# Kernel optimization log

Hardware: AMD Instinct MI355X
Metric: run time of the kernel (lower is better)

## Reference

```python
import jax, jax.numpy as jnp
import numpy as np
from jax import lax

DIM = 128
HEADS = 8
GROUPS = 8
DIM_HEAD = 64
DOWN = 4
OFF_SCALE = 4.0
KSIZE = 6
B, N, M = 2, 1024, 1024


def ln(x, g, b, eps=1e-5):
    m = x.mean(-1, keepdims=True)
    v = ((x - m) ** 2).mean(-1, keepdims=True)
    return (x - m) / jnp.sqrt(v + eps) * g + b


def grid_sample_1d(feats, grid):
    # feats: (Bg, C, Mk), grid: (Bg, Nd) normalized coords in [-1, 1]
    # bilinear, padding_mode='zeros', align_corners=False (torch semantics)
    Bg, C, Mk = feats.shape
    x = ((grid + 1.0) * Mk - 1.0) / 2.0
    x0 = jnp.floor(x)
    w1 = x - x0

    def gather(xi):
        valid = ((xi >= 0) & (xi <= Mk - 1)).astype(feats.dtype)
        idx = jnp.clip(xi, 0, Mk - 1).astype(jnp.int32)
        vals = jnp.take_along_axis(
            feats, jnp.broadcast_to(idx[:, None, :], (Bg, C, idx.shape[-1])), axis=2)
        return vals * valid[:, None, :]

    return gather(x0) * (1.0 - w1)[:, None, :] + gather(x0 + 1.0) * w1[:, None, :]


def deform_cross_attn(xq, xkv, qw, kw, vw, ow, ob, o1w, o1b, o2w,
                      c1w, c1b, c2w, c2b, c3w, c3b):
    # xq, xkv: (B, C, N) channel-first token streams
    Bb, C, Nq = xq.shape
    cg = C // GROUPS  # 16 channels per offset group
    q = jnp.einsum('bgcn,goc->bgon', xq.reshape(Bb, GROUPS, cg, Nq), qw)  # (B,g,64,N)
    gq = q.reshape(Bb * GROUPS, DIM_HEAD, Nq)
    pad = (KSIZE - DOWN) // 2
    off = lax.conv_general_dilated(gq, o1w[:, None, :], (DOWN,), [(pad, pad)],
                                   feature_group_count=DIM_HEAD,
                                   dimension_numbers=('NCH', 'OIH', 'NCH')) + o1b[None, :, None]
    off = jax.nn.gelu(off, approximate=False)
    off = jnp.tanh(jnp.einsum('bcn,c->bn', off, o2w)) * OFF_SCALE  # (B*g, Nd)
    Nd = off.shape[-1]
    vgrid = jnp.arange(Nd, dtype=off.dtype)[None] + off
    vgs = 2.0 * vgrid / max(Nd - 1, 1) - 1.0  # normalized sample positions
    xkv_g = xkv.reshape(Bb, GROUPS, cg, xkv.shape[-1]).reshape(Bb * GROUPS, cg, xkv.shape[-1])
    kv = grid_sample_1d(xkv_g, vgs).reshape(Bb, GROUPS, cg, Nd)
    k = jnp.einsum('bgcn,goc->bgon', kv, kw)
    v = jnp.einsum('bgcn,goc->bgon', kv, vw)
    sim = jnp.einsum('bhdi,bhdj->bhij', q * (DIM_HEAD ** -0.5), k)  # heads == groups
    seq = 2.0 * jnp.arange(Nq, dtype=vgs.dtype) / max(Nq - 1, 1) - 1.0
    rel = seq[None, :, None] - vgs[:, None, :]  # (B*g, N, Nd)
    bias = jnp.sign(rel) * jnp.log1p(jnp.abs(rel))
    h = jax.nn.relu(bias[..., None] * c1w[0] + c1b)  # CPB MLP, hidden=dim//4=32
    h = jax.nn.relu(h @ c2w + c2b)
    h = (h @ c3w + c3b)[..., 0]
    sim = sim + h.reshape(Bb, GROUPS, Nq, Nd)  # heads // offset_groups == 1
    attn = jax.nn.softmax(sim, axis=-1)
    out = jnp.einsum('bhij,bhdj->bhdi', attn, v).reshape(Bb, GROUPS * DIM_HEAD, Nq)
    out = jnp.einsum('bcn,oc->bon', out, ow) + ob[:, None]
    return out, attn


def mha(q_in, kv_in, w_in, b_in, w_out, b_out):
    # seq-first torch nn.MultiheadAttention, eval mode (no dropout)
    E = DIM; h = HEADS; dh = E // h
    q = q_in @ w_in[:E].T + b_in[:E]
    k = kv_in @ w_in[E:2 * E].T + b_in[E:2 * E]
    v = kv_in @ w_in[2 * E:].T + b_in[2 * E:]
    Lq, Bb, _ = q.shape
    Lk = k.shape[0]
    qh = q.reshape(Lq, Bb, h, dh).transpose(1, 2, 0, 3)
    kh = k.reshape(Lk, Bb, h, dh).transpose(1, 2, 0, 3)
    vh = v.reshape(Lk, Bb, h, dh).transpose(1, 2, 0, 3)
    attn = jax.nn.softmax(jnp.einsum('bhid,bhjd->bhij', qh, kh) * (dh ** -0.5), axis=-1)
    out = jnp.einsum('bhij,bhjd->bhid', attn, vh).transpose(2, 0, 1, 3).reshape(Lq, Bb, E)
    return out @ w_out.T + b_out


def transfusion(x1, x2, ng, nb, inw, inb, ow, ob, pw, pb):
    x = x1 + mha(ln(x1, ng, nb), ln(x2, ng, nb), inw, inb, ow, ob)
    x = ln(x.transpose(1, 0, 2), ng, nb)  # (B, N, E)
    return jnp.tanh(x.mean(1) @ pw.T + pb)[:, None, :]  # (B, 1, E)


def setup_inputs():
    key = jax.random.key(0)
    ks = iter(jax.random.split(key, 40))
    rn = lambda shape, s=0.05: jax.random.normal(next(ks), shape, dtype=jnp.float32) * s
    return {
        'x1_0': rn((B, N, DIM), 1.0),
        'x1_1': rn((B, N, DIM), 1.0),
        'x2': rn((B, M, DIM), 1.0),
        'norm_g': jnp.ones((DIM,), jnp.float32),
        'norm_b': jnp.zeros((DIM,), jnp.float32),
        'd_qw': rn((2, GROUPS, DIM_HEAD, DIM // GROUPS)),
        'd_kw': rn((2, GROUPS, DIM_HEAD, DIM // GROUPS)),
        'd_vw': rn((2, GROUPS, DIM_HEAD, DIM // GROUPS)),
        'd_ow': rn((2, DIM, GROUPS * DIM_HEAD)),
        'd_ob': jnp.zeros((2, DIM), jnp.float32),
        'd_off1w': rn((2, DIM_HEAD, KSIZE)),
        'd_off1b': jnp.zeros((2, DIM_HEAD), jnp.float32),
        'd_off2w': rn((2, DIM_HEAD)),
        'd_cpb_w1': rn((2, 1, 32)),
        'd_cpb_b1': jnp.zeros((2, 32), jnp.float32),
        'd_cpb_w2': rn((2, 32, 32)),
        'd_cpb_b2': jnp.zeros((2, 32), jnp.float32),
        'd_cpb_w3': rn((2, 32, 1)),
        'd_cpb_b3': jnp.zeros((2, 1), jnp.float32),
        'fus_w': rn((DIM, 2 * DIM)),
        'fus_b': jnp.zeros((DIM,), jnp.float32),
        'tf_ng': jnp.ones((2, DIM), jnp.float32),
        'tf_nb': jnp.zeros((2, DIM), jnp.float32),
        'tf_inw': rn((2, 3 * DIM, DIM)),
        'tf_inb': jnp.zeros((2, 3 * DIM), jnp.float32),
        'tf_ow': rn((2, DIM, DIM)),
        'tf_ob': jnp.zeros((2, DIM), jnp.float32),
        'tf_pw': rn((2, DIM, DIM)),
        'tf_pb': jnp.zeros((2, DIM), jnp.float32),
        'attn_dim': 128,
    }


def reference(x1_0, x1_1, x2, norm_g, norm_b, d_qw, d_kw, d_vw, d_ow, d_ob,
              d_off1w, d_off1b, d_off2w, d_cpb_w1, d_cpb_b1, d_cpb_w2, d_cpb_b2,
              d_cpb_w3, d_cpb_b3, fus_w, fus_b, tf_ng, tf_nb, tf_inw, tf_inb,
              tf_ow, tf_ob, tf_pw, tf_pb, attn_dim):
    nkv = ln(x2, norm_g, norm_b).transpose(0, 2, 1)
    xo1, a1 = deform_cross_attn(ln(x1_0, norm_g, norm_b).transpose(0, 2, 1), nkv,
                                d_qw[0], d_kw[0], d_vw[0], d_ow[0], d_ob[0],
                                d_off1w[0], d_off1b[0], d_off2w[0],
                                d_cpb_w1[0], d_cpb_b1[0], d_cpb_w2[0], d_cpb_b2[0],
                                d_cpb_w3[0], d_cpb_b3[0])
    xo2, a2 = deform_cross_attn(ln(x1_1, norm_g, norm_b).transpose(0, 2, 1), nkv,
                                d_qw[1], d_kw[1], d_vw[1], d_ow[1], d_ob[1],
                                d_off1w[1], d_off1b[1], d_off2w[1],
                                d_cpb_w1[1], d_cpb_b1[1], d_cpb_w2[1], d_cpb_b2[1],
                                d_cpb_w3[1], d_cpb_b3[1])
    xout1 = x1_0 + xo1.transpose(0, 2, 1)
    xout2 = x1_1 + xo2.transpose(0, 2, 1)
    x = jnp.concatenate([xout1, xout2], axis=-1) @ fus_w.T + fus_b
    query = ln(x, norm_g, norm_b).transpose(1, 0, 2)
    kv1 = ln(x1_0[:, :1, :], norm_g, norm_b).transpose(1, 0, 2)
    kv2 = ln(x1_1[:, :1, :], norm_g, norm_b).transpose(1, 0, 2)
    f1 = transfusion(query, kv1, tf_ng[0], tf_nb[0], tf_inw[0], tf_inb[0],
                     tf_ow[0], tf_ob[0], tf_pw[0], tf_pb[0])
    f2 = transfusion(query, kv2, tf_ng[1], tf_nb[1], tf_inw[1], tf_inb[1],
                     tf_ow[1], tf_ob[1], tf_pw[1], tf_pb[1])
    return (f1, f2, a1, a2)
```

## Files before the change

kernel.cpp:

```cpp
#include <hip/hip_runtime.h>
#include <hip/hip_bf16.h>


namespace {

constexpr int kN  = 1024;
constexpr int kC  = 128;
constexpr int kG  = 8;
constexpr int kDH = 64;
constexpr int kND = 256;

constexpr int   kNT    = 2048;
constexpr float kRLO   = -2.0625f;
constexpr float kRSPAN = 4.125f;

constexpr size_t W_LNKV = 0;
constexpr size_t W_LNQ1 = 262144;
constexpr size_t W_LNQ2 = 524288;
constexpr size_t W_Q    = 786432;
constexpr size_t W_K    = 1835008;
constexpr size_t W_VT   = 2097152;
constexpr size_t W_VGS  = 2359296;
constexpr size_t W_AO   = 2367488;
constexpr size_t W_TAB  = 5251072;
constexpr size_t W_MOUT = 5283844;
constexpr size_t W_PART = 5284356;
constexpr size_t W_OWB  = 5317124;
constexpr size_t W_FWB  = 5382660;

}

typedef __attribute__((ext_vector_type(8))) short short8;
typedef __attribute__((ext_vector_type(4))) float floatx4;

__device__ __forceinline__ float wave_sum(float v) {
#pragma unroll
  for (int o = 32; o > 0; o >>= 1) v += __shfl_xor(v, o, 64);
  return v;
}
__device__ __forceinline__ float cpb_lds(const float* __restrict__ tabL,
                                         float seq, float vg) {
  float rel = seq - vg;
  float ft = (rel - kRLO) * ((float)kNT / kRSPAN);
  ft = fminf(fmaxf(ft, 0.f), (float)kNT - 0.001f);
  int ix = (int)ft;
  float fw = ft - (float)ix;
  return tabL[ix] * (1.f - fw) + tabL[ix + 1] * fw;
}

__global__ void k_prep(const float* __restrict__ ow, const float* __restrict__ fw,
                       __hip_bfloat16* __restrict__ owb, __hip_bfloat16* __restrict__ fwb,
                       const float* __restrict__ x1_0, const float* __restrict__ x1_1,
                       const float* __restrict__ x2, float* __restrict__ lnq1,
                       float* __restrict__ lnq2, float* __restrict__ lnkv,
                       const float* __restrict__ ng, const float* __restrict__ nb,
                       const float* __restrict__ cw1, const float* __restrict__ cb1,
                       const float* __restrict__ cw2, const float* __restrict__ cb2,
                       const float* __restrict__ cw3, const float* __restrict__ cb3,
                       float* __restrict__ tab,
                       const float* __restrict__ tfng, const float* __restrict__ tfnb,
                       const float* __restrict__ inw, const float* __restrict__ inb,
                       const float* __restrict__ tow, const float* __restrict__ tob,
                       float* __restrict__ mout) {
  int bx = blockIdx.x;
  int t = threadIdx.x;
  if (bx < 640) {
    int id = bx * 256 + t;
    if (id < 131072) owb[id] = __float2bfloat16(ow[id]);
    else fwb[id - 131072] = __float2bfloat16(fw[id - 131072]);
  } else if (bx < 2176) {
    int w = t >> 6, lane = t & 63;
    int gr = (bx - 640) * 4 + w;
    int sel = gr >> 11, row = gr & 2047;
    const float* in = (sel == 0) ? x1_0 : (sel == 1) ? x1_1 : x2;
    float* out = (sel == 0) ? lnq1 : (sel == 1) ? lnq2 : lnkv;
    const float* xr = in + (size_t)row * kC;
    float xa = xr[lane], xb = xr[lane + 64];
    float m = wave_sum(xa + xb) * (1.f / kC);
    float da = xa - m, db = xb - m;
    float v = wave_sum(da * da + db * db) * (1.f / kC);
    float r = rsqrtf(v + 1e-5f);
    float* orow = out + (size_t)row * kC;
    orow[lane]      = da * r * ng[lane] + nb[lane];
    orow[lane + 64] = db * r * ng[lane + 64] + nb[lane + 64];
  } else if (bx < 2194) {
    int rel = bx - 2176;
    int idx = rel / 9, bb = rel - idx * 9;
    int tt = bb * 256 + t;
    if (tt <= kNT) {
      float rel_ = kRLO + (kRSPAN / (float)kNT) * (float)tt;
      float u = (rel_ >= 0.f ? 1.f : -1.f) * log1pf(fabsf(rel_));
      const float* W1 = cw1 + idx * 32; const float* B1 = cb1 + idx * 32;
      const float* W2 = cw2 + idx * 1024; const float* B2 = cb2 + idx * 32;
      const float* W3 = cw3 + idx * 32; const float* B3 = cb3 + idx;
      float h1[32];
#pragma unroll
      for (int m = 0; m < 32; ++m) h1[m] = fmaxf(0.f, u * W1[m] + B1[m]);
      float o = B3[0];
      for (int m = 0; m < 32; ++m) {
        float a = B2[m];
#pragma unroll
        for (int k = 0; k < 32; ++k) a += h1[k] * W2[k * 32 + m];
        o += fmaxf(a, 0.f) * W3[m];
      }
      tab[(size_t)idx * (kNT + 1) + tt] = o;
    }
  } else {
    int rel = bx - 2194;
    int i = rel >> 1, b = rel & 1;
    bool act = t < 128;
    __shared__ float red[2];
    __shared__ float s1[128];
    __shared__ float s2[128];
    const float* xs = (i ? x1_1 : x1_0) + (size_t)b * kN * kC;
    float x = act ? xs[t] : 0.f;
    float s = wave_sum(x);
    if (act && (t & 63) == 0) red[t >> 6] = s;
    __syncthreads();
    float m1 = (red[0] + red[1]) * (1.f / kC);
    __syncthreads();
    float d1 = x - m1;
    float ss = wave_sum(act ? d1 * d1 : 0.f);
    if (act && (t & 63) == 0) red[t >> 6] = ss;
    __syncthreads();
    float v1 = (red[0] + red[1]) * (1.f / kC);
    __syncthreads();
    float t0 = act ? d1 * rsqrtf(v1 + 1e-5f) * ng[t] + nb[t] : 0.f;
    s = wave_sum(t0);
    if (act && (t & 63) == 0) red[t >> 6] = s;
    __syncthreads();
    float m2 = (red[0] + red[1]) * (1.f / kC);
    __syncthreads();
    float d2 = t0 - m2;
    ss = wave_sum(act ? d2 * d2 : 0.f);
    if (act && (t & 63) == 0) red[t >> 6] = ss;
    __syncthreads();
    float v2 = (red[0] + red[1]) * (1.f / kC);
    if (act) s1[t] = d2 * rsqrtf(v2 + 1e-5f) * tfng[i * kC + t] + tfnb[i * kC + t];
    __syncthreads();
    if (act) {
      float a0 = 0.f;
      const float* wr = inw + (size_t)i * 384 * kC + (size_t)(256 + t) * kC;
      for (int c = 0; c < 128; ++c) a0 += s1[c] * wr[c];
      s2[t] = inb[i * 384 + 256 + t] + a0;
    }
    __syncthreads();
    if (act) {
      float a0 = 0.f;
      const float* wr2 = tow + (size_t)i * kC * kC + (size_t)t * kC;
      for (int c = 0; c < 128; ++c) a0 += s2[c] * wr2[c];
      mout[rel * kC + t] = tob[i * kC + t] + a0;
    }
  }
}

__global__ void k_qoff(const float* __restrict__ lnq1, const float* __restrict__ lnq2,
                       const float* __restrict__ qw, const float* __restrict__ o1w,
                       const float* __restrict__ o1b, const float* __restrict__ o2w,
                       __hip_bfloat16* __restrict__ qout, float* __restrict__ vgs) {
  int bx = blockIdx.x;
  if (bx < 512) {
    int bg = bx >> 4, r0 = (bx & 15) * 64;
    int str = bg >> 4, b = (bg >> 3) & 1, g = bg & 7;
    int rl = threadIdx.x & 63, dq = threadIdx.x >> 6;
    const float* lnq = str ? lnq2 : lnq1;
    const float* xr = lnq + ((size_t)(b * kN + r0 + rl)) * kC + g * 16;
    float4 x0 = *(const float4*)(xr + 0);
    float4 x1 = *(const float4*)(xr + 4);
    float4 x2 = *(const float4*)(xr + 8);
    float4 x3 = *(const float4*)(xr + 12);
    const float* wqb = qw + (size_t)str * 8192 + (size_t)g * 1024;
    __hip_bfloat16* qrow = qout + ((size_t)bg * 1024 + r0 + rl) * 64 + dq * 16;
#pragma unroll 4
    for (int dd = 0; dd < 16; ++dd) {
      int d = dq * 16 + dd;
      const float* wq = wqb + d * 16;
      float4 w0 = *(const float4*)(wq + 0);
      float4 w1 = *(const float4*)(wq + 4);
      float4 w2 = *(const float4*)(wq + 8);
      float4 w3 = *(const float4*)(wq + 12);
      float q = x0.x * w0.x + x0.y * w0.y + x0.z * w0.z + x0.w * w0.w
              + x1.x * w1.x + x1.y * w1.y + x1.z * w1.z + x1.w * w1.w
              + x2.x * w2.x + x2.y * w2.y + x2.z * w2.z + x2.w * w2.w
              + x3.x * w3.x + x3.y * w3.y + x3.z * w3.z + x3.w * w3.w;
      qrow[dd] = __float2bfloat16(q);
    }
  } else {
    int bxo = bx - 512;
    int w = threadIdx.x >> 6, lane = threadIdx.x & 63;
    int bg = bxo >> 6, j = ((bxo & 63) << 2) + w;
    int str = bg >> 4, b = (bg >> 3) & 1, g = bg & 7;
    const float* lnq = str ? lnq2 : lnq1;
    __shared__ float xr[4][96];
    int base = j * 4 - 1;
#pragma unroll
    for (int rep = 0; rep < 2; ++rep) {
      int idx = lane + rep * 64;
      if (idx < 96) {
        int r = idx >> 4, c = idx & 15, n = base + r;
        xr[w][idx] = (n >= 0 && n < kN)
                         ? lnq[((size_t)(b * kN + n)) * kC + g * 16 + c] : 0.f;
      }
    }
    const float* wq = qw + (size_t)str * 8192 + (size_t)(g * kDH + lane) * 16;
    float acc = o1b[str * 64 + lane];
#pragma unroll
    for (int k2 = 0; k2 < 6; ++k2) {
      float qv = 0.f;
#pragma unroll
      for (int c = 0; c < 16; ++c) qv += xr[w][k2 * 16 + c] * wq[c];
      acc += qv * o1w[str * 384 + lane * 6 + k2];
    }
    float ge = 0.5f * acc * (1.f + erff(acc * 0.70710678118654752440f));
    float s = wave_sum(ge * o2w[str * 64 + lane]);
    if (lane == 0)
      vgs[bg * kND + j] = 2.f * ((float)j + tanhf(s) * 4.0f) / 255.f - 1.f;
  }
}

__global__ void k_sample_kv(const float* __restrict__ lnkv, const float* __restrict__ vgs,
                            const float* __restrict__ kw, const float* __restrict__ vw,
                            __hip_bfloat16* __restrict__ kout,
                            __hip_bfloat16* __restrict__ vtout) {
  int w = threadIdx.x >> 6, lane = threadIdx.x & 63;
  int bg = blockIdx.x >> 6, j = ((blockIdx.x & 63) << 2) + w;
  int str = bg >> 4, b = (bg >> 3) & 1, g = bg & 7;
  __shared__ float sc[4][16];
  if (lane < 16) {
    float gr = vgs[bg * kND + j];
    float x = ((gr + 1.f) * 1024.f - 1.f) * 0.5f;
    float x0f = floorf(x);
    float w1 = x - x0f;
    int x0 = (int)x0f, x1 = x0 + 1;
    const float* src = lnkv + (size_t)b * kN * kC + g * 16 + lane;
    float v0 = (x0 >= 0 && x0 < 1024) ? src[(size_t)x0 * kC] : 0.f;
    float v1 = (x1 >= 0 && x1 < 1024) ? src[(size_t)x1 * kC] : 0.f;
    sc[w][lane] = v0 * (1.f - w1) + v1 * w1;
  }
  const float* kwr = kw + (size_t)str * 8192 + (size_t)(g * kDH + lane) * 16;
  const float* vwr = vw + (size_t)str * 8192 + (size_t)(g * kDH + lane) * 16;
  float ka = 0.f, va = 0.f;
#pragma unroll
  for (int c = 0; c < 16; ++c) { ka += sc[w][c] * kwr[c]; va += sc[w][c] * vwr[c]; }
  kout[((size_t)bg * 256 + j) * 64 + lane] = __float2bfloat16(ka);
  vtout[((size_t)bg * 64 + lane) * 256 + j] = __float2bfloat16(va);
}

__global__ void __launch_bounds__(256, 2)
k_attn(const __hip_bfloat16* __restrict__ q_g, const __hip_bfloat16* __restrict__ k_g,
       const __hip_bfloat16* __restrict__ vt_g, const float* __restrict__ vgs,
       const float* __restrict__ tab, float* __restrict__ aout,
       __hip_bfloat16* __restrict__ attout) {
  int bg = blockIdx.x >> 4, tile = blockIdx.x & 15;
  int str = bg >> 4;
  int i0 = tile * 64;
  int t = threadIdx.x;
  int w = t >> 6, l = t & 63;
  int lr = l & 15, lg = l >> 4;

  __shared__ __align__(16) __hip_bfloat16 Qs[64 * 72];
  __shared__ __align__(16) __hip_bfloat16 Ss[64 * 72];
  __shared__ __align__(16) __hip_bfloat16 Ps[64 * 264];

  const float* tabs = tab + str * (kNT + 1);

  {
    int r = t >> 2, c0 = (t & 3) * 16;
    const __hip_bfloat16* src = q_g + ((size_t)bg * 1024 + i0 + r) * 64 + c0;
    *(float4*)&Qs[r * 72 + c0]     = *(const float4*)src;
    *(float4*)&Qs[r * 72 + c0 + 8] = *(const float4*)(src + 8);
  }
  short8 a0 = *(const short8*)&Qs[(w * 16 + lr) * 72 + lg * 8];
  short8 a1 = *(const short8*)&Qs[(w * 16 + lr) * 72 + 32 + lg * 8];
  __syncthreads();
  float* tabL = (float*)Qs;
  for (int e = t; e <= kNT; e += 256) tabL[e] = tabs[e];

  floatx4 acc[16];
#pragma unroll
  for (int f = 0; f < 16; ++f) acc[f] = {0.f, 0.f, 0.f, 0.f};

#pragma unroll
  for (int jc = 0; jc < 4; ++jc) {
    __syncthreads();
    {
      int r = t >> 2, c0 = (t & 3) * 16;
      const __hip_bfloat16* src = k_g + ((size_t)bg * 256 + jc * 64 + r) * 64 + c0;
      *(float4*)&Ss[r * 72 + c0]     = *(const float4*)src;
      *(float4*)&Ss[r * 72 + c0 + 8] = *(const float4*)(src + 8);
    }
    __syncthreads();
#pragma unroll
    for (int ct = 0; ct < 4; ++ct) {
      short8 b0 = *(const short8*)&Ss[(ct * 16 + lr) * 72 + lg * 8];
      short8 b1 = *(const short8*)&Ss[(ct * 16 + lr) * 72 + 32 + lg * 8];
      acc[jc * 4 + ct] =
          __builtin_amdgcn_mfma_f32_16x16x32_bf16(a0, b0, acc[jc * 4 + ct], 0, 0, 0);
      acc[jc * 4 + ct] =
          __builtin_amdgcn_mfma_f32_16x16x32_bf16(a1, b1, acc[jc * 4 + ct], 0, 0, 0);
    }
  }

  float vgl[16];
#pragma unroll
  for (int f = 0; f < 16; ++f) vgl[f] = vgs[bg * 256 + f * 16 + lr];
  float* aoutb = aout + (size_t)str * 4194304 + (size_t)(bg & 15) * 262144;
#pragma unroll
  for (int reg = 0; reg < 4; ++reg) {
    int row = w * 16 + lg * 4 + reg;
    int i = i0 + row;
    float seq = 2.f * (float)i / 1023.f - 1.f;
    float sv[16];
#pragma unroll
    for (int f = 0; f < 16; ++f)
      sv[f] = acc[f][reg] * 0.125f + cpb_lds(tabL, seq, vgl[f]);
    float m = sv[0];
#pragma unroll
    for (int f = 1; f < 16; ++f) m = fmaxf(m, sv[f]);
    m = fmaxf(m, __shfl_xor(m, 1, 64));
    m = fmaxf(m, __shfl_xor(m, 2, 64));
    m = fmaxf(m, __shfl_xor(m, 4, 64));
    m = fmaxf(m, __shfl_xor(m, 8, 64));
    float ev[16], sum = 0.f;
#pragma unroll
    for (int f = 0; f < 16; ++f) { ev[f] = expf(sv[f] - m); sum += ev[f]; }
    sum += __shfl_xor(sum, 1, 64);
    sum += __shfl_xor(sum, 2, 64);
    sum += __shfl_xor(sum, 4, 64);
    sum += __shfl_xor(sum, 8, 64);
    float inv = 1.f / sum;
    float* arow = aoutb + (size_t)i * 256;
#pragma unroll
    for (int f = 0; f < 16; ++f) {
      float p = ev[f] * inv;
      arow[f * 16 + lr] = p;
      Ps[row * 264 + f * 16 + lr] = __float2bfloat16(p);
    }
  }

  floatx4 oacc[4];
#pragma unroll
  for (int dt = 0; dt < 4; ++dt) oacc[dt] = {0.f, 0.f, 0.f, 0.f};
#pragma unroll
  for (int jc = 0; jc < 4; ++jc) {
    __syncthreads();
    {
      int r = t >> 2, c0 = (t & 3) * 16;
      const __hip_bfloat16* src = vt_g + ((size_t)bg * 64 + r) * 256 + jc * 64 + c0;
      *(float4*)&Ss[r * 72 + c0]     = *(const float4*)src;
      *(float4*)&Ss[r * 72 + c0 + 8] = *(const float4*)(src + 8);
    }
    __syncthreads();
    short8 pa0 = *(const short8*)&Ps[(w * 16 + lr) * 264 + jc * 64 + lg * 8];
    short8 pa1 = *(const short8*)&Ps[(w * 16 + lr) * 264 + jc * 64 + 32 + lg * 8];
#pragma unroll
    for (int dt = 0; dt < 4; ++dt) {
      short8 b0 = *(const short8*)&Ss[(dt * 16 + lr) * 72 + lg * 8];
      short8 b1 = *(const short8*)&Ss[(dt * 16 + lr) * 72 + 32 + lg * 8];
      oacc[dt] = __builtin_amdgcn_mfma_f32_16x16x32_bf16(pa0, b0, oacc[dt], 0, 0, 0);
      oacc[dt] = __builtin_amdgcn_mfma_f32_16x16x32_bf16(pa1, b1, oacc[dt], 0, 0, 0);
    }
  }
  {
    int b = (bg >> 3) & 1, g = bg & 7;
    __hip_bfloat16* ab = attout + ((size_t)(str * 2 + b) * 1024) * 512 + (size_t)g * 64;
#pragma unroll
    for (int dt = 0; dt < 4; ++dt)
#pragma unroll
      for (int reg = 0; reg < 4; ++reg) {
        int row = w * 16 + lg * 4 + reg;
        ab[(size_t)(i0 + row) * 512 + dt * 16 + lr] = __float2bfloat16(oacc[dt][reg]);
      }
  }
}

__global__ void __launch_bounds__(256, 2)
k_oproj_fuse(const __hip_bfloat16* __restrict__ aog, const __hip_bfloat16* __restrict__ owb,
             const float* __restrict__ ob,
             const float* __restrict__ x1_0, const float* __restrict__ x1_1,
             const __hip_bfloat16* __restrict__ fwb, const float* __restrict__ fb,
             const float* __restrict__ ng, const float* __restrict__ nb,
             const float* __restrict__ tfng, const float* __restrict__ tfnb,
             const float* __restrict__ mout, float* __restrict__ partial) {
  int tok0 = blockIdx.x * 16;
  int t = threadIdx.x;
  int w = t >> 6, l = t & 63;
  int lr = l & 15, lg = l >> 4;
  int nt0 = w * 2;

  __shared__ __align__(16) unsigned char smem[16 * 280 * 2];
  __shared__ float red[4][128];
  __hip_bfloat16* xos = (__hip_bfloat16*)smem;
  float* fs = (float*)smem;

  for (int s = 0; s < 2; ++s) {
    const __hip_bfloat16* arow = aog + ((size_t)(s * 2048 + tok0 + lr)) * 512 + lg * 8;
    const __hip_bfloat16* wb0 = owb + (size_t)s * 65536 + (size_t)((nt0 + 0) * 16 + lr) * 512 + lg * 8;
    const __hip_bfloat16* wb1 = owb + (size_t)s * 65536 + (size_t)((nt0 + 1) * 16 + lr) * 512 + lg * 8;
    floatx4 acc0 = {0.f, 0.f, 0.f, 0.f}, acc1 = {0.f, 0.f, 0.f, 0.f};
#pragma unroll
    for (int ks = 0; ks < 16; ++ks) {
      short8 a  = *(const short8*)(arow + ks * 32);
      short8 b0 = *(const short8*)(wb0 + ks * 32);
      short8 b1 = *(const short8*)(wb1 + ks * 32);
      acc0 = __builtin_amdgcn_mfma_f32_16x16x32_bf16(a, b0, acc0, 0, 0, 0);
      acc1 = __builtin_amdgcn_mfma_f32_16x16x32_bf16(a, b1, acc1, 0, 0, 0);
    }
    const float* x1 = s ? x1_1 : x1_0;
    float bias0 = ob[s * 128 + nt0 * 16 + lr];
    float bias1 = ob[s * 128 + (nt0 + 1) * 16 + lr];
#pragma unroll
    for (int reg = 0; reg < 4; ++reg) {
      int row = lg * 4 + reg;
      size_t xi = (size_t)(tok0 + row) * 128;
      xos[row * 280 + s * 128 + nt0 * 16 + lr] =
          __float2bfloat16(acc0[reg] + x1[xi + nt0 * 16 + lr] + bias0);
      xos[row * 280 + s * 128 + (nt0 + 1) * 16 + lr] =
          __float2bfloat16(acc1[reg] + x1[xi + (nt0 + 1) * 16 + lr] + bias1);
    }
  }
  __syncthreads();

  floatx4 f0 = {0.f, 0.f, 0.f, 0.f}, f1 = {0.f, 0.f, 0.f, 0.f};
  const __hip_bfloat16* fb0 = fwb + (size_t)((nt0 + 0) * 16 + lr) * 256 + lg * 8;
  const __hip_bfloat16* fb1 = fwb + (size_t)((nt0 + 1) * 16 + lr) * 256 + lg * 8;
#pragma unroll
  for (int ks = 0; ks < 8; ++ks) {
    short8 a  = *(const short8*)&xos[lr * 280 + ks * 32 + lg * 8];
    short8 b0 = *(const short8*)(fb0 + ks * 32);
    short8 b1 = *(const short8*)(fb1 + ks * 32);
    f0 = __builtin_amdgcn_mfma_f32_16x16x32_bf16(a, b0, f0, 0, 0, 0);
    f1 = __builtin_amdgcn_mfma_f32_16x16x32_bf16(a, b1, f1, 0, 0, 0);
  }
  __syncthreads();

  {
    float fbias0 = fb[nt0 * 16 + lr], fbias1 = fb[(nt0 + 1) * 16 + lr];
#pragma unroll
    for (int reg = 0; reg < 4; ++reg) {
      int row = lg * 4 + reg;
      fs[row * 132 + w * 32 + lr]      = f0[reg] + fbias0;
      fs[row * 132 + w * 32 + 16 + lr] = f1[reg] + fbias1;
    }
  }
  __syncthreads();

  int b = tok0 >> 10, chunk = (tok0 & 1023) >> 4;
  float g1a = ng[l], b1a = nb[l], g1b = ng[l + 64], b1b = nb[l + 64];
  float mo0a = mout[b * 128 + l], mo0b = mout[b * 128 + l + 64];
  float mo1a = mout[(2 + b) * 128 + l], mo1b = mout[(2 + b) * 128 + l + 64];
  float g20a = tfng[l], b20a = tfnb[l], g20b = tfng[l + 64], b20b = tfnb[l + 64];
  float g21a = tfng[128 + l], b21a = tfnb[128 + l];
  float g21b = tfng[192 + l], b21b = tfnb[192 + l];
  float acc0a = 0.f, acc0b = 0.f, acc1a = 0.f, acc1b = 0.f;
#pragma unroll
  for (int it = 0; it < 4; ++it) {
    int tok = it * 4 + w;
    float xa = fs[tok * 132 + l], xb = fs[tok * 132 + l + 64];
    float m1 = wave_sum(xa + xb) * (1.f / kC);
    float da = xa - m1, db = xb - m1;
    float v1 = wave_sum(da * da + db * db) * (1.f / kC);
    float r1 = rsqrtf(v1 + 1e-5f);
    float ba = da * r1 * g1a + b1a, bb = db * r1 * g1b + b1b;
    {
      float za = ba + mo0a, zb = bb + mo0b;
      float m2 = wave_sum(za + zb) * (1.f / kC);
      float ea = za - m2, eb = zb - m2;
      float v2 = wave_sum(ea * ea + eb * eb) * (1.f / kC);
      float r2 = rsqrtf(v2 + 1e-5f);
      acc0a += ea * r2 * g20a + b20a;
      acc0b += eb * r2 * g20b + b20b;
    }
    {
      float za = ba + mo1a, zb = bb + mo1b;
      float m2 = wave_sum(za + zb) * (1.f / kC);
      float ea = za - m2, eb = zb - m2;
      float v2 = wave_sum(ea * ea + eb * eb) * (1.f / kC);
      float r2 = rsqrtf(v2 + 1e-5f);
      acc1a += ea * r2 * g21a + b21a;
      acc1b += eb * r2 * g21b + b21b;
    }
  }
  red[w][l] = acc0a; red[w][l + 64] = acc0b;
  __syncthreads();
  if (w == 0) {
    float* pr = partial + ((size_t)(b)*64 + chunk) * kC;
    pr[l]      = red[0][l] + red[1][l] + red[2][l] + red[3][l];
    pr[l + 64] = red[0][l + 64] + red[1][l + 64] + red[2][l + 64] + red[3][l + 64];
  }
  __syncthreads();
  red[w][l] = acc1a; red[w][l + 64] = acc1b;
  __syncthreads();
  if (w == 0) {
    float* pr = partial + ((size_t)(2 + b) * 64 + chunk) * kC;
    pr[l]      = red[0][l] + red[1][l] + red[2][l] + red[3][l];
    pr[l + 64] = red[0][l + 64] + red[1][l + 64] + red[2][l + 64] + red[3][l + 64];
  }
}

__global__ void k_final(const float* __restrict__ partial, const float* __restrict__ pw,
                        const float* __restrict__ pb, float* __restrict__ out) {
  int ib = blockIdx.x;
  int i = ib >> 1, t = threadIdx.x;
  int c = t & 127, half = t >> 7;
  float a = 0.f;
  for (int ch = half * 32; ch < half * 32 + 32; ++ch)
    a += partial[((size_t)ib * 64 + ch) * kC + c];
  __shared__ float s[256];
  s[half * 128 + c] = a;
  __syncthreads();
  if (t < 128) s[t] = (s[t] + s[128 + t]) * (1.f / (float)kN);
  __syncthreads();
  if (t < 128) {
    float a0 = 0.f;
    const float* wr = pw + (size_t)i * kC * kC + (size_t)t * kC;
    for (int cc = 0; cc < 128; ++cc) a0 += s[cc] * wr[cc];
    out[ib * 128 + t] = tanhf(pb[i * kC + t] + a0);
  }
}

extern "C" void kernel_launch(void* const* d_in, const int* in_sizes, int n_in,
                              void* d_out, int out_size, void* d_ws, size_t ws_size,
                              hipStream_t stream) {
  const float* x1_0   = (const float*)d_in[0];
  const float* x1_1   = (const float*)d_in[1];
  const float* x2     = (const float*)d_in[2];
  const float* norm_g = (const float*)d_in[3];
  const float* norm_b = (const float*)d_in[4];
  const float* d_qw   = (const float*)d_in[5];
  const float* d_kw   = (const float*)d_in[6];
  const float* d_vw   = (const float*)d_in[7];
  const float* d_ow   = (const float*)d_in[8];
  const float* d_ob   = (const float*)d_in[9];
  const float* d_o1w  = (const float*)d_in[10];
  const float* d_o1b  = (const float*)d_in[11];
  const float* d_o2w  = (const float*)d_in[12];
  const float* c_w1   = (const float*)d_in[13];
  const float* c_b1   = (const float*)d_in[14];
  const float* c_w2   = (const float*)d_in[15];
  const float* c_b2   = (const float*)d_in[16];
  const float* c_w3   = (const float*)d_in[17];
  const float* c_b3   = (const float*)d_in[18];
  const float* fus_w  = (const float*)d_in[19];
  const float* fus_b  = (const float*)d_in[20];
  const float* tf_ng  = (const float*)d_in[21];
  const float* tf_nb  = (const float*)d_in[22];
  const float* tf_inw = (const float*)d_in[23];
  const float* tf_inb = (const float*)d_in[24];
  const float* tf_ow  = (const float*)d_in[25];
  const float* tf_ob  = (const float*)d_in[26];
  const float* tf_pw  = (const float*)d_in[27];
  const float* tf_pb  = (const float*)d_in[28];

  float* ws = (float*)d_ws;
  float* out = (float*)d_out;
  float* lnkv = ws + W_LNKV;
  float* lnq1 = ws + W_LNQ1; float* lnq2 = ws + W_LNQ2;
  __hip_bfloat16* qb  = (__hip_bfloat16*)(ws + W_Q);
  __hip_bfloat16* kb  = (__hip_bfloat16*)(ws + W_K);
  __hip_bfloat16* vtb = (__hip_bfloat16*)(ws + W_VT);
  float* vgsw = ws + W_VGS;
  __hip_bfloat16* aob = (__hip_bfloat16*)(ws + W_AO);
  float* tab = ws + W_TAB;
  float* moutp = ws + W_MOUT; float* partp = ws + W_PART;
  __hip_bfloat16* owb = (__hip_bfloat16*)(ws + W_OWB);
  __hip_bfloat16* fwb = (__hip_bfloat16*)(ws + W_FWB);

  float* aoutb = out + 512;

  k_prep<<<2198, 256, 0, stream>>>(d_ow, fus_w, owb, fwb,
                                   x1_0, x1_1, x2, lnq1, lnq2, lnkv, norm_g, norm_b,
                                   c_w1, c_b1, c_w2, c_b2, c_w3, c_b3, tab,
                                   tf_ng, tf_nb, tf_inw, tf_inb, tf_ow, tf_ob, moutp);
  k_qoff<<<2560, 256, 0, stream>>>(lnq1, lnq2, d_qw, d_o1w, d_o1b, d_o2w, qb, vgsw);
  k_sample_kv<<<2048, 256, 0, stream>>>(lnkv, vgsw, d_kw, d_vw, kb, vtb);
  k_attn<<<512, 256, 0, stream>>>(qb, kb, vtb, vgsw, tab, aoutb, aob);
  k_oproj_fuse<<<128, 256, 0, stream>>>(aob, owb, d_ob, x1_0, x1_1, fwb, fus_b,
                                        norm_g, norm_b, tf_ng, tf_nb, moutp, partp);
  k_final<<<4, 256, 0, stream>>>(partp, tf_pw, tf_pb, out);

  (void)in_sizes; (void)n_in; (void)out_size; (void)ws_size;
}
```

Before: 88.61 us.

## Stage full K and V tiles in LDS, prefetch V during softmax

```diff
diff --git a/kernel.cpp b/kernel.cpp
--- a/kernel.cpp
+++ b/kernel.cpp
@@ -38,14 +38,14 @@
   for (int o = 32; o > 0; o >>= 1) v += __shfl_xor(v, o, 64);
   return v;
 }
-__device__ __forceinline__ float cpb_lds(const float* __restrict__ tabL,
-                                         float seq, float vg) {
+__device__ __forceinline__ float cpb_bias(const float* __restrict__ tabs,
+                                          float seq, float vg) {
   float rel = seq - vg;
   float ft = (rel - kRLO) * ((float)kNT / kRSPAN);
   ft = fminf(fmaxf(ft, 0.f), (float)kNT - 0.001f);
   int ix = (int)ft;
   float fw = ft - (float)ix;
-  return tabL[ix] * (1.f - fw) + tabL[ix + 1] * fw;
+  return tabs[ix] * (1.f - fw) + tabs[ix + 1] * fw;
 }
 
 __global__ void k_prep(const float* __restrict__ ow, const float* __restrict__ fw,
@@ -259,46 +259,55 @@
   int lr = l & 15, lg = l >> 4;
 
   __shared__ __align__(16) __hip_bfloat16 Qs[64 * 72];
-  __shared__ __align__(16) __hip_bfloat16 Ss[64 * 72];
+  __shared__ __align__(16) __hip_bfloat16 KVs[256 * 72];
   __shared__ __align__(16) __hip_bfloat16 Ps[64 * 264];
 
   const float* tabs = tab + str * (kNT + 1);
 
   {
-    int r = t >> 2, c0 = (t & 3) * 16;
-    const __hip_bfloat16* src = q_g + ((size_t)bg * 1024 + i0 + r) * 64 + c0;
-    *(float4*)&Qs[r * 72 + c0]     = *(const float4*)src;
-    *(float4*)&Qs[r * 72 + c0 + 8] = *(const float4*)(src + 8);
-  }
+    const __hip_bfloat16* qflat = q_g + ((size_t)bg * 1024 + i0) * 64;
+#pragma unroll
+    for (int i2 = 0; i2 < 2; ++i2) {
+      int e = i2 * 2048 + t * 8;
+      int r = e >> 6, c = e & 63;
+      *(float4*)&Qs[r * 72 + c] = *(const float4*)(qflat + e);
+    }
+    const __hip_bfloat16* kflat = k_g + (size_t)bg * 256 * 64;
+#pragma unroll
+    for (int i2 = 0; i2 < 8; ++i2) {
+      int e = i2 * 2048 + t * 8;
+      int r = e >> 6, c = e & 63;
+      *(float4*)&KVs[r * 72 + c] = *(const float4*)(kflat + e);
+    }
+  }
+  __syncthreads();
+
   short8 a0 = *(const short8*)&Qs[(w * 16 + lr) * 72 + lg * 8];
   short8 a1 = *(const short8*)&Qs[(w * 16 + lr) * 72 + 32 + lg * 8];
-  __syncthreads();
-  float* tabL = (float*)Qs;
-  for (int e = t; e <= kNT; e += 256) tabL[e] = tabs[e];
 
   floatx4 acc[16];
 #pragma unroll
   for (int f = 0; f < 16; ++f) acc[f] = {0.f, 0.f, 0.f, 0.f};
-
-#pragma unroll
-  for (int jc = 0; jc < 4; ++jc) {
-    __syncthreads();
-    {
-      int r = t >> 2, c0 = (t & 3) * 16;
-      const __hip_bfloat16* src = k_g + ((size_t)bg * 256 + jc * 64 + r) * 64 + c0;
-      *(float4*)&Ss[r * 72 + c0]     = *(const float4*)src;
-      *(float4*)&Ss[r * 72 + c0 + 8] = *(const float4*)(src + 8);
-    }
-    __syncthreads();
-#pragma unroll
-    for (int ct = 0; ct < 4; ++ct) {
-      short8 b0 = *(const short8*)&Ss[(ct * 16 + lr) * 72 + lg * 8];
-      short8 b1 = *(const short8*)&Ss[(ct * 16 + lr) * 72 + 32 + lg * 8];
-      acc[jc * 4 + ct] =
-          __builtin_amdgcn_mfma_f32_16x16x32_bf16(a0, b0, acc[jc * 4 + ct], 0, 0, 0);
-      acc[jc * 4 + ct] =
-          __builtin_amdgcn_mfma_f32_16x16x32_bf16(a1, b1, acc[jc * 4 + ct], 0, 0, 0);
-    }
+#pragma unroll
+  for (int ct = 0; ct < 16; ++ct) {
+    short8 b0 = *(const short8*)&KVs[(ct * 16 + lr) * 72 + lg * 8];
+    short8 b1 = *(const short8*)&KVs[(ct * 16 + lr) * 72 + 32 + lg * 8];
+    acc[ct] = __builtin_amdgcn_mfma_f32_16x16x32_bf16(a0, b0, acc[ct], 0, 0, 0);
+    acc[ct] = __builtin_amdgcn_mfma_f32_16x16x32_bf16(a1, b1, acc[ct], 0, 0, 0);
+  }
+  __syncthreads();
+
+  float4 vr0, vr1, vr2, vr3, vr4, vr5, vr6, vr7;
+  {
+    const __hip_bfloat16* vflat = vt_g + (size_t)bg * 64 * 256;
+    vr0 = *(const float4*)(vflat + 0 * 2048 + t * 8);
+    vr1 = *(const float4*)(vflat + 1 * 2048 + t * 8);
+    vr2 = *(const float4*)(vflat + 2 * 2048 + t * 8);
+    vr3 = *(const float4*)(vflat + 3 * 2048 + t * 8);
+    vr4 = *(const float4*)(vflat + 4 * 2048 + t * 8);
+    vr5 = *(const float4*)(vflat + 5 * 2048 + t * 8);
+    vr6 = *(const float4*)(vflat + 6 * 2048 + t * 8);
+    vr7 = *(const float4*)(vflat + 7 * 2048 + t * 8);
   }
 
   float vgl[16];
@@ -313,7 +322,7 @@
     float sv[16];
 #pragma unroll
     for (int f = 0; f < 16; ++f)
-      sv[f] = acc[f][reg] * 0.125f + cpb_lds(tabL, seq, vgl[f]);
+      sv[f] = acc[f][reg] * 0.125f + cpb_bias(tabs, seq, vgl[f]);
     float m = sv[0];
 #pragma unroll
     for (int f = 1; f < 16; ++f) m = fmaxf(m, sv[f]);
@@ -323,7 +332,7 @@
     m = fmaxf(m, __shfl_xor(m, 8, 64));
     float ev[16], sum = 0.f;
 #pragma unroll
-    for (int f = 0; f < 16; ++f) { ev[f] = expf(sv[f] - m); sum += ev[f]; }
+    for (int f = 0; f < 16; ++f) { ev[f] = __expf(sv[f] - m); sum += ev[f]; }
     sum += __shfl_xor(sum, 1, 64);
     sum += __shfl_xor(sum, 2, 64);
     sum += __shfl_xor(sum, 4, 64);
@@ -338,27 +347,30 @@
     }
   }
 
+  {
+    int e0 = t * 8;
+#pragma unroll
+    for (int i2 = 0; i2 < 8; ++i2) {
+      int e = i2 * 2048 + e0;
+      int r = e >> 8, c = e & 255;
+      float4 v = (i2 == 0) ? vr0 : (i2 == 1) ? vr1 : (i2 == 2) ? vr2 :
+                 (i2 == 3) ? vr3 : (i2 == 4) ? vr4 : (i2 == 5) ? vr5 :
+                 (i2 == 6) ? vr6 : vr7;
+      *(float4*)&KVs[r * 264 + c] = v;
+    }
+  }
+  __syncthreads();
+
   floatx4 oacc[4];
 #pragma unroll
   for (int dt = 0; dt < 4; ++dt) oacc[dt] = {0.f, 0.f, 0.f, 0.f};
 #pragma unroll
-  for (int jc = 0; jc < 4; ++jc) {
-    __syncthreads();
-    {
-      int r = t >> 2, c0 = (t & 3) * 16;
-      const __hip_bfloat16* src = vt_g + ((size_t)bg * 64 + r) * 256 + jc * 64 + c0;
-      *(float4*)&Ss[r * 72 + c0]     = *(const float4*)src;
-      *(float4*)&Ss[r * 72 + c0 + 8] = *(const float4*)(src + 8);
-    }
-    __syncthreads();
-    short8 pa0 = *(const short8*)&Ps[(w * 16 + lr) * 264 + jc * 64 + lg * 8];
-    short8 pa1 = *(const short8*)&Ps[(w * 16 + lr) * 264 + jc * 64 + 32 + lg * 8];
+  for (int ks = 0; ks < 8; ++ks) {
+    short8 pa = *(const short8*)&Ps[(w * 16 + lr) * 264 + ks * 32 + lg * 8];
 #pragma unroll
     for (int dt = 0; dt < 4; ++dt) {
-      short8 b0 = *(const short8*)&Ss[(dt * 16 + lr) * 72 + lg * 8];
-      short8 b1 = *(const short8*)&Ss[(dt * 16 + lr) * 72 + 32 + lg * 8];
-      oacc[dt] = __builtin_amdgcn_mfma_f32_16x16x32_bf16(pa0, b0, oacc[dt], 0, 0, 0);
-      oacc[dt] = __builtin_amdgcn_mfma_f32_16x16x32_bf16(pa1, b1, oacc[dt], 0, 0, 0);
+      short8 b = *(const short8*)&KVs[(dt * 16 + lr) * 264 + ks * 32 + lg * 8];
+      oacc[dt] = __builtin_amdgcn_mfma_f32_16x16x32_bf16(pa, b, oacc[dt], 0, 0, 0);
     }
   }
   {
```

Measured after the change: 83.29 us. -6.0%, faster.
